# Kernel optimization log

Measured on AMD Instinct MI355X. Metric: run time of the kernel, lower is better.

Reference implementation:

```python
import jax, jax.numpy as jnp
import numpy as np

QMAX_W = 127.0   # symmetric int8 for weights
QMAX_A = 255.0   # asymmetric uint8 for activations


def setup_inputs() -> dict:
    key = jax.random.key(0)
    k1, k2, k3 = jax.random.split(key, 3)
    B, S, K, N = 4, 2048, 4096, 4096
    x = jax.random.normal(k1, (B, S, K), dtype=jnp.float32)
    weight = jax.random.normal(k2, (N, K), dtype=jnp.float32) * (1.0 / np.sqrt(K))
    bias = jax.random.normal(k3, (N,), dtype=jnp.float32) * 0.02
    return {"x": x, "weight": weight, "bias": bias}


def reference(x, weight, bias):
    N, K = weight.shape
    # --- weight quantization: row-wise symmetric int8 (absmax / 127) ---
    row_absmax = jnp.max(jnp.abs(weight), axis=1)            # [N]
    row_scales = jnp.where(row_absmax > 0, row_absmax / QMAX_W, 1.0)
    Wq = jnp.clip(jnp.round(weight / row_scales[:, None]), -QMAX_W, QMAX_W)  # int8 values, kept f32 for GEMM

    # --- activation quantization: per-token (column of X^T) asymmetric uint8 ---
    orig_shape = x.shape
    X = x.reshape(-1, K)                                     # [M, K]
    xmin = jnp.min(X, axis=1)                                # [M]
    xmax = jnp.max(X, axis=1)
    rng = xmax - xmin
    col_scales = jnp.where(rng > 0, rng / QMAX_A, 1.0)       # [M]
    col_zps = jnp.round(-xmin / col_scales)                  # [M]
    Xq = jnp.clip(jnp.round(X / col_scales[:, None]) + col_zps[:, None], 0.0, QMAX_A)  # uint8 values

    # --- int GEMM with zero-point correction + dequant: Y[m,n] = s_a[m]*s_w[n]*sum_k (Xq-zp)[m,k]*Wq[n,k] ---
    acc = jnp.einsum('mk,nk->mn', Xq - col_zps[:, None], Wq)  # [M, N]
    Y = acc * (col_scales[:, None] * row_scales[None, :]) + bias
    return Y.reshape(orig_shape[:-1] + (N,))
```

## Files before the change

### kernel.cpp

```cpp
#include <hip/hip_runtime.h>
#include <stdint.h>
#include <stddef.h>

typedef __attribute__((ext_vector_type(4))) int i32x4;

#define BM 128
#define BN 128
#define BK 64

__device__ __forceinline__ void gload_lds16(const void* g, void* l) {
    __builtin_amdgcn_global_load_lds(
        (const __attribute__((address_space(1))) void*)g,
        (__attribute__((address_space(3))) void*)l,
        16, 0, 0);
}

__device__ __forceinline__ float waveAllMaxF(float v) {
#pragma unroll
    for (int m = 32; m > 0; m >>= 1) v = fmaxf(v, __shfl_xor(v, m, 64));
    return v;
}
__device__ __forceinline__ float waveAllMinF(float v) {
#pragma unroll
    for (int m = 32; m > 0; m >>= 1) v = fminf(v, __shfl_xor(v, m, 64));
    return v;
}
__device__ __forceinline__ int waveAllSumI(int v) {
#pragma unroll
    for (int m = 32; m > 0; m >>= 1) v += __shfl_xor(v, m, 64);
    return v;
}

__global__ void __launch_bounds__(256) wquant_kernel(
    const float* __restrict__ W, int8_t* __restrict__ Wq,
    float* __restrict__ rscale, int* __restrict__ rsum, int K) {
    const int n = blockIdx.x * 4 + (threadIdx.x >> 6);
    const int lane = threadIdx.x & 63;
    const float4* row = (const float4*)(W + (size_t)n * K);
    int* out = (int*)(Wq + (size_t)n * K);

    if (K == 4096) {
        float4 v[16];
#pragma unroll
        for (int j = 0; j < 16; ++j) v[j] = row[lane + (j << 6)];

        float amax = 0.f;
#pragma unroll
        for (int j = 0; j < 16; ++j) {
            amax = fmaxf(amax, fmaxf(fmaxf(fabsf(v[j].x), fabsf(v[j].y)),
                                     fmaxf(fabsf(v[j].z), fabsf(v[j].w))));
        }
        amax = waveAllMaxF(amax);
        const float scale = (amax > 0.f) ? (amax / 127.0f) : 1.0f;

        int lsum = 0;
#pragma unroll
        for (int j = 0; j < 16; ++j) {
            int q0 = (int)fminf(fmaxf(rintf(v[j].x / scale), -127.f), 127.f);
            int q1 = (int)fminf(fmaxf(rintf(v[j].y / scale), -127.f), 127.f);
            int q2 = (int)fminf(fmaxf(rintf(v[j].z / scale), -127.f), 127.f);
            int q3 = (int)fminf(fmaxf(rintf(v[j].w / scale), -127.f), 127.f);
            lsum += q0 + q1 + q2 + q3;
            out[lane + (j << 6)] =
                (q0 & 255) | ((q1 & 255) << 8) | ((q2 & 255) << 16) | ((q3 & 255) << 24);
        }
        lsum = waveAllSumI(lsum);
        if (lane == 0) { rsum[n] = lsum; rscale[n] = scale; }
    } else {
        const int K4 = K >> 2;
        float amax = 0.f;
        for (int i = lane; i < K4; i += 64) {
            float4 f = row[i];
            amax = fmaxf(amax, fmaxf(fmaxf(fabsf(f.x), fabsf(f.y)),
                                     fmaxf(fabsf(f.z), fabsf(f.w))));
        }
        amax = waveAllMaxF(amax);
        const float scale = (amax > 0.f) ? (amax / 127.0f) : 1.0f;
        int lsum = 0;
        for (int i = lane; i < K4; i += 64) {
            float4 f = row[i];
            int q0 = (int)fminf(fmaxf(rintf(f.x / scale), -127.f), 127.f);
            int q1 = (int)fminf(fmaxf(rintf(f.y / scale), -127.f), 127.f);
            int q2 = (int)fminf(fmaxf(rintf(f.z / scale), -127.f), 127.f);
            int q3 = (int)fminf(fmaxf(rintf(f.w / scale), -127.f), 127.f);
            lsum += q0 + q1 + q2 + q3;
            out[i] = (q0 & 255) | ((q1 & 255) << 8) | ((q2 & 255) << 16) | ((q3 & 255) << 24);
        }
        lsum = waveAllSumI(lsum);
        if (lane == 0) { rsum[n] = lsum; rscale[n] = scale; }
    }
}

__global__ void __launch_bounds__(256) aquant_kernel(
    const float* __restrict__ X, int8_t* __restrict__ Xq,
    float* __restrict__ cscale, int* __restrict__ azp, int K) {
    const int m = blockIdx.x * 4 + (threadIdx.x >> 6);
    const int lane = threadIdx.x & 63;
    const float4* row = (const float4*)(X + (size_t)m * K);
    int* out = (int*)(Xq + (size_t)m * K);

    if (K == 4096) {
        float4 v[16];
#pragma unroll
        for (int j = 0; j < 16; ++j) v[j] = row[lane + (j << 6)];

        float vmin = 3.402823466e38f, vmax = -3.402823466e38f;
#pragma unroll
        for (int j = 0; j < 16; ++j) {
            vmin = fminf(vmin, fminf(fminf(v[j].x, v[j].y), fminf(v[j].z, v[j].w)));
            vmax = fmaxf(vmax, fmaxf(fmaxf(v[j].x, v[j].y), fmaxf(v[j].z, v[j].w)));
        }
        vmin = waveAllMinF(vmin);
        vmax = waveAllMaxF(vmax);

        const float rng = vmax - vmin;
        const float scale = (rng > 0.f) ? (rng / 255.0f) : 1.0f;
        const float zp = rintf(-vmin / scale);

#pragma unroll
        for (int j = 0; j < 16; ++j) {
            int q0 = (int)fminf(fmaxf(rintf(v[j].x / scale) + zp, 0.f), 255.f) - 128;
            int q1 = (int)fminf(fmaxf(rintf(v[j].y / scale) + zp, 0.f), 255.f) - 128;
            int q2 = (int)fminf(fmaxf(rintf(v[j].z / scale) + zp, 0.f), 255.f) - 128;
            int q3 = (int)fminf(fmaxf(rintf(v[j].w / scale) + zp, 0.f), 255.f) - 128;
            out[lane + (j << 6)] =
                (q0 & 255) | ((q1 & 255) << 8) | ((q2 & 255) << 16) | ((q3 & 255) << 24);
        }
        if (lane == 0) { cscale[m] = scale; azp[m] = 128 - (int)zp; }
    } else {
        const int K4 = K >> 2;
        float vmin = 3.402823466e38f, vmax = -3.402823466e38f;
        for (int i = lane; i < K4; i += 64) {
            float4 f = row[i];
            vmin = fminf(vmin, fminf(fminf(f.x, f.y), fminf(f.z, f.w)));
            vmax = fmaxf(vmax, fmaxf(fmaxf(f.x, f.y), fmaxf(f.z, f.w)));
        }
        vmin = waveAllMinF(vmin);
        vmax = waveAllMaxF(vmax);
        const float rng = vmax - vmin;
        const float scale = (rng > 0.f) ? (rng / 255.0f) : 1.0f;
        const float zp = rintf(-vmin / scale);
        for (int i = lane; i < K4; i += 64) {
            float4 f = row[i];
            int q0 = (int)fminf(fmaxf(rintf(f.x / scale) + zp, 0.f), 255.f) - 128;
            int q1 = (int)fminf(fmaxf(rintf(f.y / scale) + zp, 0.f), 255.f) - 128;
            int q2 = (int)fminf(fmaxf(rintf(f.z / scale) + zp, 0.f), 255.f) - 128;
            int q3 = (int)fminf(fmaxf(rintf(f.w / scale) + zp, 0.f), 255.f) - 128;
            out[i] = (q0 & 255) | ((q1 & 255) << 8) | ((q2 & 255) << 16) | ((q3 & 255) << 24);
        }
        if (lane == 0) { cscale[m] = scale; azp[m] = 128 - (int)zp; }
    }
}

__global__ void __launch_bounds__(256) gemm_i8_kernel(
    const int8_t* __restrict__ A, const int8_t* __restrict__ B,
    float* __restrict__ Y,
    const float* __restrict__ cs, const int* __restrict__ azp,
    const float* __restrict__ rs, const int* __restrict__ rsum,
    const float* __restrict__ bias, int M, int N, int K) {
    __shared__ int8_t As[BM * BK];
    __shared__ int8_t Bs[BN * BK];

    const int tid = threadIdx.x;
    const int lane = tid & 63;
    const int wave = tid >> 6;
    const int wm = wave & 1;
    const int wn = wave >> 1;
    const int quad = lane >> 4;
    const int lr = lane & 15;

    const int bm = blockIdx.x * BM;
    const int bn = blockIdx.y * BN;

    const int8_t* Ag = A + (size_t)bm * K;
    const int8_t* Bg = B + (size_t)bn * K;

    const int srow = tid >> 2;
    const int scol = (tid & 3) << 4;

    i32x4 acc[4][4] = {};

    for (int k0 = 0; k0 < K; k0 += BK) {
        gload_lds16(Ag + (size_t)srow * K + (k0 + scol), &As[srow * BK + scol]);
        gload_lds16(Ag + (size_t)(srow + 64) * K + (k0 + scol), &As[(srow + 64) * BK + scol]);
        gload_lds16(Bg + (size_t)srow * K + (k0 + scol), &Bs[srow * BK + scol]);
        gload_lds16(Bg + (size_t)(srow + 64) * K + (k0 + scol), &Bs[(srow + 64) * BK + scol]);
        __syncthreads();

        i32x4 af[4], bf[4];
#pragma unroll
        for (int i = 0; i < 4; ++i)
            af[i] = *(const i32x4*)&As[(wm * 64 + i * 16 + lr) * BK + quad * 16];
#pragma unroll
        for (int j = 0; j < 4; ++j)
            bf[j] = *(const i32x4*)&Bs[(wn * 64 + j * 16 + lr) * BK + quad * 16];

#pragma unroll
        for (int i = 0; i < 4; ++i)
#pragma unroll
            for (int j = 0; j < 4; ++j)
                acc[i][j] = __builtin_amdgcn_mfma_i32_16x16x64_i8(af[i], bf[j], acc[i][j], 0, 0, 0);

        __syncthreads();
    }

#pragma unroll
    for (int i = 0; i < 4; ++i) {
        const int mb = bm + wm * 64 + i * 16 + quad * 4;
#pragma unroll
        for (int r = 0; r < 4; ++r) {
            const int m = mb + r;
            const float csm = cs[m];
            const int az = azp[m];
            float* yrow = Y + (size_t)m * N;
#pragma unroll
            for (int j = 0; j < 4; ++j) {
                const int n = bn + wn * 64 + j * 16 + lr;
                const int tot = acc[i][j][r] + az * rsum[n];
                yrow[n] = fmaf((float)tot, csm * rs[n], bias[n]);
            }
        }
    }
}

extern "C" void kernel_launch(void* const* d_in, const int* in_sizes, int n_in,
                              void* d_out, int out_size, void* d_ws, size_t ws_size,
                              hipStream_t stream) {
    const float* x = (const float*)d_in[0];
    const float* w = (const float*)d_in[1];
    const float* bias = (const float*)d_in[2];
    float* y = (float*)d_out;

    const int N = in_sizes[2];
    const int K = in_sizes[1] / N;
    const int M = in_sizes[0] / K;

    uint8_t* ws = (uint8_t*)d_ws;
    int8_t* Wq = (int8_t*)ws;
    int8_t* Xq = (int8_t*)(ws + (size_t)N * K);
    uint8_t* p = ws + (size_t)N * K + (size_t)M * K;
    p = (uint8_t*)(((uintptr_t)p + 255) & ~(uintptr_t)255);
    float* rscale = (float*)p;  p += (size_t)N * sizeof(float);
    int*   rsum   = (int*)p;    p += (size_t)N * sizeof(int);
    float* cscale = (float*)p;  p += (size_t)M * sizeof(float);
    int*   azp    = (int*)p;    p += (size_t)M * sizeof(int);

    wquant_kernel<<<N / 4, 256, 0, stream>>>(w, Wq, rscale, rsum, K);
    aquant_kernel<<<M / 4, 256, 0, stream>>>(x, Xq, cscale, azp, K);

    dim3 grid(M / BM, N / BN);
    gemm_i8_kernel<<<grid, 256, 0, stream>>>(Xq, Wq, y, cscale, azp,
                                             rscale, rsum, bias, M, N, K);
}
```

Before: 501.6 us.

## Enlarge int8 GEMM tiles to 256x256 with double-buffered swizzled LDS

Rewrites the int8 MFMA GEMM to use 256x256 output tiles with BK=128 across 8 waves, each wave holding an 8x4 grid of accumulators. Global-to-LDS loads go into a double buffer (128KB of dynamic shared memory), so the next K tile is fetched while the current one is computed. An XOR swizzle on the LDS column slots is meant to avoid bank conflicts on the fragment reads. Workgroup IDs are remapped across XCDs to improve L2 locality. The cost is higher register and LDS pressure, which limits the CU to one block and reduces latency hiding from occupancy.

```diff
diff --git a/kernel.cpp b/kernel.cpp
--- a/kernel.cpp
+++ b/kernel.cpp
@@ -3,10 +3,6 @@
 #include <stddef.h>
 
 typedef __attribute__((ext_vector_type(4))) int i32x4;
-
-#define BM 128
-#define BN 128
-#define BK 64
 
 __device__ __forceinline__ void gload_lds16(const void* g, void* l) {
     __builtin_amdgcn_global_load_lds(
@@ -152,61 +148,97 @@
     }
 }
 
-__global__ void __launch_bounds__(256) gemm_i8_kernel(
+__global__ void __launch_bounds__(512, 2) gemm_i8_kernel(
     const int8_t* __restrict__ A, const int8_t* __restrict__ B,
     float* __restrict__ Y,
     const float* __restrict__ cs, const int* __restrict__ azp,
     const float* __restrict__ rs, const int* __restrict__ rsum,
     const float* __restrict__ bias, int M, int N, int K) {
-    __shared__ int8_t As[BM * BK];
-    __shared__ int8_t Bs[BN * BK];
+    extern __shared__ int8_t smem[];
 
     const int tid = threadIdx.x;
     const int lane = tid & 63;
     const int wave = tid >> 6;
-    const int wm = wave & 1;
-    const int wn = wave >> 1;
+    const int wm = wave >> 2;
+    const int wn = wave & 3;
     const int quad = lane >> 4;
     const int lr = lane & 15;
 
-    const int bm = blockIdx.x * BM;
-    const int bn = blockIdx.y * BN;
+    const int nwg = gridDim.x * gridDim.y;
+    int wid = blockIdx.y * gridDim.x + blockIdx.x;
+    if ((nwg & 7) == 0) wid = (wid & 7) * (nwg >> 3) + (wid >> 3);
+    const int bm = (wid % gridDim.x) * 256;
+    const int bn = (wid / gridDim.x) * 256;
 
     const int8_t* Ag = A + (size_t)bm * K;
     const int8_t* Bg = B + (size_t)bn * K;
 
-    const int srow = tid >> 2;
-    const int scol = (tid & 3) << 4;
-
-    i32x4 acc[4][4] = {};
-
-    for (int k0 = 0; k0 < K; k0 += BK) {
-        gload_lds16(Ag + (size_t)srow * K + (k0 + scol), &As[srow * BK + scol]);
-        gload_lds16(Ag + (size_t)(srow + 64) * K + (k0 + scol), &As[(srow + 64) * BK + scol]);
-        gload_lds16(Bg + (size_t)srow * K + (k0 + scol), &Bs[srow * BK + scol]);
-        gload_lds16(Bg + (size_t)(srow + 64) * K + (k0 + scol), &Bs[(srow + 64) * BK + scol]);
+    const int sr = tid >> 3;
+    const int sc = tid & 7;
+    const int csrc = (sc ^ (sr & 7)) << 4;
+
+    i32x4 acc[8][4] = {};
+
+    const int NT = K >> 7;
+
+    {
+        int8_t* dA = smem;
+        int8_t* dB = smem + 32768;
+#pragma unroll
+        for (int q = 0; q < 4; ++q) {
+            const int r = q * 64 + sr;
+            gload_lds16(Ag + (size_t)r * K + csrc, dA + r * 128 + (sc << 4));
+            gload_lds16(Bg + (size_t)r * K + csrc, dB + r * 128 + (sc << 4));
+        }
+    }
+    __syncthreads();
+
+    int buf = 0;
+    for (int t = 0; t < NT; ++t) {
+        if (t + 1 < NT) {
+            const int k0 = (t + 1) << 7;
+            int8_t* dA = smem + (buf ^ 1) * 65536;
+            int8_t* dB = dA + 32768;
+#pragma unroll
+            for (int q = 0; q < 4; ++q) {
+                const int r = q * 64 + sr;
+                gload_lds16(Ag + (size_t)r * K + (k0 + csrc), dA + r * 128 + (sc << 4));
+                gload_lds16(Bg + (size_t)r * K + (k0 + csrc), dB + r * 128 + (sc << 4));
+            }
+        }
+
+        const int8_t* Ab = smem + buf * 65536;
+        const int8_t* Bb = Ab + 32768;
+        const int axor = lr & 7;
+#pragma unroll
+        for (int kk = 0; kk < 2; ++kk) {
+            i32x4 af[8], bf[4];
+#pragma unroll
+            for (int i = 0; i < 8; ++i) {
+                const int row = wm * 128 + i * 16 + lr;
+                const int slot = ((kk << 2) | quad) ^ axor;
+                af[i] = *(const i32x4*)&Ab[row * 128 + (slot << 4)];
+            }
+#pragma unroll
+            for (int j = 0; j < 4; ++j) {
+                const int row = wn * 64 + j * 16 + lr;
+                const int slot = ((kk << 2) | quad) ^ axor;
+                bf[j] = *(const i32x4*)&Bb[row * 128 + (slot << 4)];
+            }
+#pragma unroll
+            for (int i = 0; i < 8; ++i)
+#pragma unroll
+                for (int j = 0; j < 4; ++j)
+                    acc[i][j] = __builtin_amdgcn_mfma_i32_16x16x64_i8(af[i], bf[j], acc[i][j], 0, 0, 0);
+        }
+
         __syncthreads();
-
-        i32x4 af[4], bf[4];
-#pragma unroll
-        for (int i = 0; i < 4; ++i)
-            af[i] = *(const i32x4*)&As[(wm * 64 + i * 16 + lr) * BK + quad * 16];
-#pragma unroll
-        for (int j = 0; j < 4; ++j)
-            bf[j] = *(const i32x4*)&Bs[(wn * 64 + j * 16 + lr) * BK + quad * 16];
-
-#pragma unroll
-        for (int i = 0; i < 4; ++i)
-#pragma unroll
-            for (int j = 0; j < 4; ++j)
-                acc[i][j] = __builtin_amdgcn_mfma_i32_16x16x64_i8(af[i], bf[j], acc[i][j], 0, 0, 0);
-
-        __syncthreads();
-    }
-
-#pragma unroll
-    for (int i = 0; i < 4; ++i) {
-        const int mb = bm + wm * 64 + i * 16 + quad * 4;
+        buf ^= 1;
+    }
+
+#pragma unroll
+    for (int i = 0; i < 8; ++i) {
+        const int mb = bm + wm * 128 + i * 16 + quad * 4;
 #pragma unroll
         for (int r = 0; r < 4; ++r) {
             const int m = mb + r;
@@ -245,10 +277,17 @@
     float* cscale = (float*)p;  p += (size_t)M * sizeof(float);
     int*   azp    = (int*)p;    p += (size_t)M * sizeof(int);
 
+    static int lds_cfg = 0;
+    if (!lds_cfg) {
+        (void)hipFuncSetAttribute((const void*)gemm_i8_kernel,
+                                  hipFuncAttributeMaxDynamicSharedMemorySize, 131072);
+        lds_cfg = 1;
+    }
+
     wquant_kernel<<<N / 4, 256, 0, stream>>>(w, Wq, rscale, rsum, K);
     aquant_kernel<<<M / 4, 256, 0, stream>>>(x, Xq, cscale, azp, K);
 
-    dim3 grid(M / BM, N / BN);
-    gemm_i8_kernel<<<grid, 256, 0, stream>>>(Xq, Wq, y, cscale, azp,
-                                             rscale, rsum, bias, M, N, K);
-}
+    dim3 grid(M / 256, N / 256);
+    gemm_i8_kernel<<<grid, 512, 131072, stream>>>(Xq, Wq, y, cscale, azp,
+                                                  rscale, rsum, bias, M, N, K);
+}
```

New measurement: 407.5 us. -18.8%, faster.
